# Kernel tuning notes

Measured on AMD Instinct MI355X. Metric: run time of the kernel, lower is better.

The kernel has to match this reference:

```python
import jax, jax.numpy as jnp
import numpy as np
from jax import lax

WINDOW = 11
SIGMA = 1.5
CHANNELS = 2
PAD = WINDOW // 2


def make_gaussian_kernel(window_size=WINDOW, sigma=SIGMA, channels=CHANNELS):
    # matches torch: range(-window_size//2 + 1, window_size//2 + 1) -> [-5..5] for 11
    xs = np.arange(-(window_size // 2), window_size // 2 + 1, dtype=np.float32)
    g = np.exp(-xs ** 2 / (2.0 * sigma ** 2))
    k2 = g[:, None] * g[None, :]
    k2 = k2 / k2.sum()
    # depthwise kernel, OIHW with I=1, O=channels
    k = np.broadcast_to(k2[None, None], (channels, 1, window_size, window_size))
    return jnp.asarray(k)


def dwconv(img, kernel):
    # depthwise 2D conv, SAME-style padding with pad = window//2
    return lax.conv_general_dilated(
        img, kernel,
        window_strides=(1, 1),
        padding=[(PAD, PAD), (PAD, PAD)],
        dimension_numbers=('NCHW', 'OIHW', 'NCHW'),
        feature_group_count=kernel.shape[0])


def setup_inputs() -> dict:
    key = jax.random.key(0)
    k1, k2 = jax.random.split(key)
    B, C, H, W = 32, CHANNELS, 512, 512
    x = jax.random.uniform(k1, (B, C, H, W), dtype=jnp.float32)
    y = jax.random.uniform(k2, (B, C, H, W), dtype=jnp.float32)
    kernel = make_gaussian_kernel()
    return {"x": x, "y": y, "kernel": kernel}


def reference(x, y, kernel):
    mu_x = dwconv(x, kernel)
    mu_y = dwconv(y, kernel)
    mu_x_sq = mu_x * mu_x
    mu_y_sq = mu_y * mu_y
    mu_xy = mu_x * mu_y
    sigma_x_sq = dwconv(x * x, kernel) - mu_x_sq
    sigma_y_sq = dwconv(y * y, kernel) - mu_y_sq
    sigma_xy = dwconv(x * y, kernel) - mu_xy
    C1 = 0.01 ** 2
    C2 = 0.03 ** 2
    ssim_map = ((2 * mu_xy + C1) * (2 * sigma_xy + C2)) / (
        (mu_x_sq + mu_y_sq + C1) * (sigma_x_sq + sigma_y_sq + C2))
    return 1.0 - jnp.mean(ssim_map)
```

## Files before the change

kernel.cpp:

```cpp
#include <hip/hip_runtime.h>

#define WIN   11
#define PADR  5
#define TILE  32
#define HALO  (TILE + WIN - 1)
#define NTHREADS 256

__global__ __launch_bounds__(NTHREADS)
void ssim_tile_kernel(const float* __restrict__ x,
                      const float* __restrict__ y,
                      const float* __restrict__ kern,
                      float* __restrict__ partial,
                      int nTiles, int H, int W)
{
    __shared__ float lds_x[HALO][HALO + 1];
    __shared__ float lds_y[HALO][HALO + 1];
    __shared__ float hbuf[5][HALO][TILE + 1];
    __shared__ float wsum[NTHREADS / 64];

    const int tid   = threadIdx.x;
    const int tilesPerPlane = nTiles * nTiles;
    const int plane = blockIdx.x / tilesPerPlane;
    const int tile  = blockIdx.x % tilesPerPlane;
    const int tr    = tile / nTiles;
    const int tc    = tile % nTiles;
    const int row0  = tr * TILE - PADR;
    const int col0  = tc * TILE - PADR;

    const float* xp = x + (size_t)plane * H * W;
    const float* yp = y + (size_t)plane * H * W;

    float w[WIN];
    {
        const float cinv = rsqrtf(kern[PADR * WIN + PADR]);
        #pragma unroll
        for (int i = 0; i < WIN; ++i)
            w[i] = kern[i * WIN + PADR] * cinv;
    }

    for (int idx = tid; idx < HALO * HALO; idx += NTHREADS) {
        const int r = idx / HALO;
        const int c = idx - r * HALO;
        const int gr = row0 + r;
        const int gc = col0 + c;
        const bool ok = (gr >= 0) & (gr < H) & (gc >= 0) & (gc < W);
        float vx = 0.f, vy = 0.f;
        if (ok) {
            vx = xp[(size_t)gr * W + gc];
            vy = yp[(size_t)gr * W + gc];
        }
        lds_x[r][c] = vx;
        lds_y[r][c] = vy;
    }
    __syncthreads();

    for (int pos = tid; pos < HALO * TILE; pos += NTHREADS) {
        const int r = pos >> 5;
        const int c = pos & 31;
        float hx = 0.f, hy = 0.f, hxx = 0.f, hyy = 0.f, hxy = 0.f;
        #pragma unroll
        for (int k = 0; k < WIN; ++k) {
            const float sx = lds_x[r][c + k];
            const float sy = lds_y[r][c + k];
            const float wk = w[k];
            hx  += wk * sx;
            hy  += wk * sy;
            hxx += wk * sx * sx;
            hyy += wk * sy * sy;
            hxy += wk * sx * sy;
        }
        hbuf[0][r][c] = hx;
        hbuf[1][r][c] = hy;
        hbuf[2][r][c] = hxx;
        hbuf[3][r][c] = hyy;
        hbuf[4][r][c] = hxy;
    }
    __syncthreads();

    const int c  = tid & 31;
    const int r0 = (tid >> 5) * 4;

    float acc[5][4];
    #pragma unroll
    for (int f = 0; f < 5; ++f)
        #pragma unroll
        for (int j = 0; j < 4; ++j)
            acc[f][j] = 0.f;

    #pragma unroll
    for (int rr = 0; rr < WIN + 3; ++rr) {
        float v[5];
        #pragma unroll
        for (int f = 0; f < 5; ++f)
            v[f] = hbuf[f][r0 + rr][c];
        #pragma unroll
        for (int j = 0; j < 4; ++j) {
            const int k = rr - j;
            if (k >= 0 && k < WIN) {
                const float wk = w[k];
                #pragma unroll
                for (int f = 0; f < 5; ++f)
                    acc[f][j] += wk * v[f];
            }
        }
    }

    const float C1 = 1e-4f;
    const float C2 = 9e-4f;
    float lsum = 0.f;
    #pragma unroll
    for (int j = 0; j < 4; ++j) {
        const float mx  = acc[0][j];
        const float my  = acc[1][j];
        const float mxx = mx * mx;
        const float myy = my * my;
        const float mxy = mx * my;
        const float sxx = acc[2][j] - mxx;
        const float syy = acc[3][j] - myy;
        const float sxy = acc[4][j] - mxy;
        const float num = (2.f * mxy + C1) * (2.f * sxy + C2);
        const float den = (mxx + myy + C1) * (sxx + syy + C2);
        lsum += num / den;
    }

    #pragma unroll
    for (int off = 32; off > 0; off >>= 1)
        lsum += __shfl_down(lsum, off, 64);
    if ((tid & 63) == 0)
        wsum[tid >> 6] = lsum;
    __syncthreads();
    if (tid == 0)
        partial[blockIdx.x] = wsum[0] + wsum[1] + wsum[2] + wsum[3];
}

__global__ __launch_bounds__(NTHREADS)
void ssim_finalize_kernel(const float* __restrict__ partial, int n,
                          float* __restrict__ out, float invN)
{
    __shared__ float wsum[NTHREADS / 64];
    float s = 0.f;
    for (int i = threadIdx.x; i < n; i += NTHREADS)
        s += partial[i];
    #pragma unroll
    for (int off = 32; off > 0; off >>= 1)
        s += __shfl_down(s, off, 64);
    if ((threadIdx.x & 63) == 0)
        wsum[threadIdx.x >> 6] = s;
    __syncthreads();
    if (threadIdx.x == 0)
        out[0] = 1.0f - (wsum[0] + wsum[1] + wsum[2] + wsum[3]) * invN;
}

extern "C" void kernel_launch(void* const* d_in, const int* in_sizes, int n_in,
                              void* d_out, int out_size, void* d_ws, size_t ws_size,
                              hipStream_t stream)
{
    const float* x    = (const float*)d_in[0];
    const float* y    = (const float*)d_in[1];
    const float* kern = (const float*)d_in[2];
    float* out = (float*)d_out;

    const int H = 512, W = 512;
    const int planes = in_sizes[0] / (H * W);
    const int nTiles = W / TILE;
    const int nBlocks = planes * nTiles * nTiles;

    float* partial = (float*)d_ws;

    ssim_tile_kernel<<<nBlocks, NTHREADS, 0, stream>>>(
        x, y, kern, partial, nTiles, H, W);

    const float invN = 1.0f / ((float)planes * H * W);
    ssim_finalize_kernel<<<1, NTHREADS, 0, stream>>>(partial, nBlocks, out, invN);
}
```

Before: 291.2 us.

## Stream full-width row chunks with register vertical pass and swizzled LDS horizontal pass

Replaces the 32x32 tiled kernel with a streaming kernel. Each block handles one full-width 66-row chunk of a plane, with each thread owning one column. The vertical 11-tap pass is done in a rotating register accumulator for the five fields, and the results go into an XOR-swizzled LDS ring buffer that the horizontal pass reads with float4 loads. This removes the 2D halo reloads and the per-tile overheads. The division becomes a fast reciprocal and the final reduction uses a single float atomicAdd, which makes summation order nondeterministic and adds a memset launch. It also uses only 512 blocks with heavy register pressure (55 accumulators), which risks low occupancy.

Result: slower. 371.2 us (+27.5%).

```diff
diff --git a/kernel.cpp b/kernel.cpp
--- a/kernel.cpp
+++ b/kernel.cpp
@@ -1,154 +1,151 @@
 #include <hip/hip_runtime.h>
 
-#define WIN   11
-#define PADR  5
-#define TILE  32
-#define HALO  (TILE + WIN - 1)
-#define NTHREADS 256
+#define WIN    11
+#define IMG    512
+#define CH     66
+#define NCHUNK 8
+#define PITCH  528
+#define FSTRIDE (WIN*PITCH)
+#define VBUF_DW (5*FSTRIDE)
+#define NT     512
 
-__global__ __launch_bounds__(NTHREADS)
-void ssim_tile_kernel(const float* __restrict__ x,
-                      const float* __restrict__ y,
-                      const float* __restrict__ kern,
-                      float* __restrict__ partial,
-                      int nTiles, int H, int W)
+__device__ __forceinline__ unsigned swz(unsigned b) {
+    return b ^ ((b >> 3) & 0x70u);
+}
+
+__global__ __launch_bounds__(NT, 2)
+void ssim_stream_kernel(const float* __restrict__ x,
+                        const float* __restrict__ y,
+                        const float* __restrict__ kern,
+                        float* __restrict__ accum)
 {
-    __shared__ float lds_x[HALO][HALO + 1];
-    __shared__ float lds_y[HALO][HALO + 1];
-    __shared__ float hbuf[5][HALO][TILE + 1];
-    __shared__ float wsum[NTHREADS / 64];
+    __shared__ float vbuf[VBUF_DW];
+    __shared__ float wsum[NT/64];
 
     const int tid   = threadIdx.x;
-    const int tilesPerPlane = nTiles * nTiles;
-    const int plane = blockIdx.x / tilesPerPlane;
-    const int tile  = blockIdx.x % tilesPerPlane;
-    const int tr    = tile / nTiles;
-    const int tc    = tile % nTiles;
-    const int row0  = tr * TILE - PADR;
-    const int col0  = tc * TILE - PADR;
+    const int plane = blockIdx.x >> 3;
+    const int chunk = blockIdx.x & 7;
+    const int r0    = chunk * CH;
 
-    const float* xp = x + (size_t)plane * H * W;
-    const float* yp = y + (size_t)plane * H * W;
+    const float* xp = x + (size_t)plane * (IMG*IMG);
+    const float* yp = y + (size_t)plane * (IMG*IMG);
 
     float w[WIN];
     {
-        const float cinv = rsqrtf(kern[PADR * WIN + PADR]);
+        const float cinv = rsqrtf(kern[5*WIN+5]);
         #pragma unroll
-        for (int i = 0; i < WIN; ++i)
-            w[i] = kern[i * WIN + PADR] * cinv;
+        for (int i = 0; i < WIN; ++i) w[i] = kern[i*WIN+5] * cinv;
     }
 
-    for (int idx = tid; idx < HALO * HALO; idx += NTHREADS) {
-        const int r = idx / HALO;
-        const int c = idx - r * HALO;
-        const int gr = row0 + r;
-        const int gc = col0 + c;
-        const bool ok = (gr >= 0) & (gr < H) & (gc >= 0) & (gc < W);
-        float vx = 0.f, vy = 0.f;
-        if (ok) {
-            vx = xp[(size_t)gr * W + gc];
-            vy = yp[(size_t)gr * W + gc];
-        }
-        lds_x[r][c] = vx;
-        lds_y[r][c] = vy;
-    }
+    for (int idx = tid; idx < VBUF_DW; idx += NT) vbuf[idx] = 0.f;
     __syncthreads();
 
-    for (int pos = tid; pos < HALO * TILE; pos += NTHREADS) {
-        const int r = pos >> 5;
-        const int c = pos & 31;
-        float hx = 0.f, hy = 0.f, hxx = 0.f, hyy = 0.f, hxy = 0.f;
-        #pragma unroll
-        for (int k = 0; k < WIN; ++k) {
-            const float sx = lds_x[r][c + k];
-            const float sy = lds_y[r][c + k];
-            const float wk = w[k];
-            hx  += wk * sx;
-            hy  += wk * sy;
-            hxx += wk * sx * sx;
-            hyy += wk * sy * sy;
-            hxy += wk * sx * sy;
-        }
-        hbuf[0][r][c] = hx;
-        hbuf[1][r][c] = hy;
-        hbuf[2][r][c] = hxx;
-        hbuf[3][r][c] = hyy;
-        hbuf[4][r][c] = hxy;
-    }
-    __syncthreads();
-
-    const int c  = tid & 31;
-    const int r0 = (tid >> 5) * 4;
-
-    float acc[5][4];
+    float acc[5][WIN];
     #pragma unroll
     for (int f = 0; f < 5; ++f)
         #pragma unroll
-        for (int j = 0; j < 4; ++j)
-            acc[f][j] = 0.f;
+        for (int s = 0; s < WIN; ++s) acc[f][s] = 0.f;
 
-    #pragma unroll
-    for (int rr = 0; rr < WIN + 3; ++rr) {
-        float v[5];
+    float lsum = 0.f;
+    char* vb = (char*)vbuf;
+
+    for (int g = 0; g < 7; ++g) {
         #pragma unroll
-        for (int f = 0; f < 5; ++f)
-            v[f] = hbuf[f][r0 + rr][c];
-        #pragma unroll
-        for (int j = 0; j < 4; ++j) {
-            const int k = rr - j;
-            if (k >= 0 && k < WIN) {
-                const float wk = w[k];
+        for (int m = 0; m < WIN; ++m) {
+            const int i = r0 - 5 + 11*g + m;
+            float vx = 0.f, vy = 0.f;
+            if ((unsigned)i < IMG) {
+                vx = xp[(size_t)i*IMG + tid];
+                vy = yp[(size_t)i*IMG + tid];
+            }
+            const float vxx = vx*vx, vyy = vy*vy, vxy = vx*vy;
+            #pragma unroll
+            for (int s = 0; s < WIN; ++s) {
+                const float wk = w[(m + WIN - s) % WIN];
+                acc[0][s] += wk * vx;
+                acc[1][s] += wk * vy;
+                acc[2][s] += wk * vxx;
+                acc[3][s] += wk * vyy;
+                acc[4][s] += wk * vxy;
+            }
+            const int cs = (m + 1) % WIN;
+            const int rl = 11*g + m - 10;
+            if (rl >= 0 && rl < CH) {
+                const int rr = rl % WIN;
+                const unsigned dbase = (unsigned)(rr*PITCH + 5 + tid);
                 #pragma unroll
-                for (int f = 0; f < 5; ++f)
-                    acc[f][j] += wk * v[f];
+                for (int f = 0; f < 5; ++f) {
+                    const unsigned byte = (dbase + f*FSTRIDE) * 4u;
+                    *(float*)(vb + swz(byte)) = acc[f][cs];
+                }
+            }
+            #pragma unroll
+            for (int f = 0; f < 5; ++f) acc[f][cs] = 0.f;
+        }
+
+        const int rllo = (g == 0) ? 0 : 11*g - 10;
+        const int rlhi = (11*g < CH) ? 11*g : CH - 1;
+        const int ntasks = (rlhi - rllo + 1) * 64;
+        __syncthreads();
+        for (int task = tid; task < ntasks; task += NT) {
+            const int o    = task & 63;
+            const int rid  = rllo + (task >> 6);
+            const int orow = r0 + rid;
+            if (orow < IMG) {
+                const int rr = rid % WIN;
+                float res[5][8];
+                #pragma unroll
+                for (int f = 0; f < 5; ++f) {
+                    float win[20];
+                    const unsigned d0 = (unsigned)(f*FSTRIDE + rr*PITCH + 8*o);
+                    #pragma unroll
+                    for (int j = 0; j < 5; ++j) {
+                        const unsigned byte = (d0 + 4u*j) * 4u;
+                        const float4 q = *(const float4*)(vb + swz(byte));
+                        win[4*j+0] = q.x; win[4*j+1] = q.y;
+                        win[4*j+2] = q.z; win[4*j+3] = q.w;
+                    }
+                    #pragma unroll
+                    for (int j = 0; j < 8; ++j) {
+                        float s = 0.f;
+                        #pragma unroll
+                        for (int k = 0; k < WIN; ++k) s += w[k] * win[j+k];
+                        res[f][j] = s;
+                    }
+                }
+                #pragma unroll
+                for (int j = 0; j < 8; ++j) {
+                    const float mx = res[0][j], my = res[1][j];
+                    const float mxx = mx*mx, myy = my*my, mxy = mx*my;
+                    const float sxx = res[2][j] - mxx;
+                    const float syy = res[3][j] - myy;
+                    const float sxy = res[4][j] - mxy;
+                    const float num = (2.f*mxy + 1e-4f) * (2.f*sxy + 9e-4f);
+                    const float den = (mxx + myy + 1e-4f) * (sxx + syy + 9e-4f);
+                    lsum += num * __builtin_amdgcn_rcpf(den);
+                }
             }
         }
-    }
-
-    const float C1 = 1e-4f;
-    const float C2 = 9e-4f;
-    float lsum = 0.f;
-    #pragma unroll
-    for (int j = 0; j < 4; ++j) {
-        const float mx  = acc[0][j];
-        const float my  = acc[1][j];
-        const float mxx = mx * mx;
-        const float myy = my * my;
-        const float mxy = mx * my;
-        const float sxx = acc[2][j] - mxx;
-        const float syy = acc[3][j] - myy;
-        const float sxy = acc[4][j] - mxy;
-        const float num = (2.f * mxy + C1) * (2.f * sxy + C2);
-        const float den = (mxx + myy + C1) * (sxx + syy + C2);
-        lsum += num / den;
+        __syncthreads();
     }
 
     #pragma unroll
     for (int off = 32; off > 0; off >>= 1)
         lsum += __shfl_down(lsum, off, 64);
-    if ((tid & 63) == 0)
-        wsum[tid >> 6] = lsum;
+    if ((tid & 63) == 0) wsum[tid >> 6] = lsum;
     __syncthreads();
-    if (tid == 0)
-        partial[blockIdx.x] = wsum[0] + wsum[1] + wsum[2] + wsum[3];
+    if (tid == 0) {
+        float s = 0.f;
+        #pragma unroll
+        for (int k = 0; k < NT/64; ++k) s += wsum[k];
+        atomicAdd(accum, s);
+    }
 }
 
-__global__ __launch_bounds__(NTHREADS)
-void ssim_finalize_kernel(const float* __restrict__ partial, int n,
-                          float* __restrict__ out, float invN)
+__global__ void ssim_finalize(const float* __restrict__ accum,
+                              float* __restrict__ out, float invN)
 {
-    __shared__ float wsum[NTHREADS / 64];
-    float s = 0.f;
-    for (int i = threadIdx.x; i < n; i += NTHREADS)
-        s += partial[i];
-    #pragma unroll
-    for (int off = 32; off > 0; off >>= 1)
-        s += __shfl_down(s, off, 64);
-    if ((threadIdx.x & 63) == 0)
-        wsum[threadIdx.x >> 6] = s;
-    __syncthreads();
-    if (threadIdx.x == 0)
-        out[0] = 1.0f - (wsum[0] + wsum[1] + wsum[2] + wsum[3]) * invN;
+    out[0] = 1.0f - accum[0] * invN;
 }
 
 extern "C" void kernel_launch(void* const* d_in, const int* in_sizes, int n_in,
@@ -158,18 +155,13 @@
     const float* x    = (const float*)d_in[0];
     const float* y    = (const float*)d_in[1];
     const float* kern = (const float*)d_in[2];
-    float* out = (float*)d_out;
+    float* out   = (float*)d_out;
+    float* accum = (float*)d_ws;
 
-    const int H = 512, W = 512;
-    const int planes = in_sizes[0] / (H * W);
-    const int nTiles = W / TILE;
-    const int nBlocks = planes * nTiles * nTiles;
+    const int planes = in_sizes[0] / (IMG*IMG);
 
-    float* partial = (float*)d_ws;
-
-    ssim_tile_kernel<<<nBlocks, NTHREADS, 0, stream>>>(
-        x, y, kern, partial, nTiles, H, W);
-
-    const float invN = 1.0f / ((float)planes * H * W);
-    ssim_finalize_kernel<<<1, NTHREADS, 0, stream>>>(partial, nBlocks, out, invN);
+    hipMemsetAsync(accum, 0, sizeof(float), stream);
+    ssim_stream_kernel<<<planes*NCHUNK, NT, 0, stream>>>(x, y, kern, accum);
+    ssim_finalize<<<1, 1, 0, stream>>>(accum, out,
+                                       1.0f / ((float)planes * IMG * IMG));
 }
```
